# Performance work log

Measured on AMD Instinct MI355X. Metric: run time of the kernel, lower is better.

Reference implementation:

```python
import jax, jax.numpy as jnp
import numpy as np

B, N, C = 2048, 64, 384
H, WS, HIDDEN, TEMB = 12, 8, 64, 384
D = C // H


def _rpb_index(ws):
    coords = np.stack(np.meshgrid(np.arange(ws), np.arange(ws), indexing='ij'))  # (2, ws, ws)
    flat = coords.reshape(2, -1)                       # (2, ws*ws)
    rel = flat[:, :, None] - flat[:, None, :]          # (2, N, N)
    rel = rel.transpose(1, 2, 0).copy()                # (N, N, 2)
    rel[..., 0] += ws - 1
    rel[..., 1] += ws - 1
    rel[..., 0] *= 2 * ws - 1
    return rel.sum(-1)                                  # (N, N) int


def setup_inputs() -> dict:
    key = jax.random.key(0)
    ks = jax.random.split(key, 16)
    s = 0.02
    inp = {
        'x': jax.random.normal(ks[0], (B, N, C), jnp.float32),
        'temb': jax.random.normal(ks[1], (B, TEMB), jnp.float32),
        'sigma': jax.random.uniform(ks[2], (B,), jnp.float32, 1e-3, 1.0),
        'qkv_w': jax.random.normal(ks[3], (C, 3 * C), jnp.float32) * s,
        'qkv_b': jax.random.normal(ks[4], (3 * C,), jnp.float32) * s,
        'qkvt_w': jax.random.normal(ks[5], (TEMB, 3 * C), jnp.float32) * s,
        'trunk_w1': jax.random.normal(ks[6], (1, HIDDEN), jnp.float32) * s,
        'trunk_b1': jax.random.normal(ks[7], (HIDDEN,), jnp.float32) * s,
        'trunk_w2': jax.random.normal(ks[8], (HIDDEN, HIDDEN), jnp.float32) * s,
        'trunk_b2': jax.random.normal(ks[9], (HIDDEN,), jnp.float32) * s,
        'gate_w': jax.random.normal(ks[10], (HIDDEN, 1), jnp.float32) * s,
        'gate_b': jnp.zeros((1,), jnp.float32),
        'bias_w': jax.random.normal(ks[11], (HIDDEN, H), jnp.float32) * s,
        'bias_b': jax.random.normal(ks[12], (H,), jnp.float32) * s,
        'proj_w': jax.random.normal(ks[13], (C, C), jnp.float32) * s,
        'proj_b': jax.random.normal(ks[14], (C,), jnp.float32) * s,
        'rpb_table': jax.random.normal(ks[15], ((2 * WS - 1) * (2 * WS - 1), H), jnp.float32) * s,
        'rpb_index': jnp.asarray(_rpb_index(WS), jnp.int32),
    }
    return inp


def reference(x, temb, sigma, qkv_w, qkv_b, qkvt_w, trunk_w1, trunk_b1,
              trunk_w2, trunk_b2, gate_w, gate_b, bias_w, bias_b,
              proj_w, proj_b, rpb_table, rpb_index):
    b, n, c = x.shape
    h, d = H, c // H
    scale = d ** -0.5
    # QKV with time-embedding modulation
    qkv = x @ qkv_w + qkv_b + (temb @ qkvt_w)[:, None, :]        # (B, N, 3C)
    qkv = qkv.reshape(b, n, 3, h, d).transpose(2, 0, 3, 1, 4)     # (3, B, H, N, D)
    q, k, v = qkv[0], qkv[1], qkv[2]
    attn = jnp.einsum('bhnd,bhmd->bhnm', q * scale, k)            # (B, H, N, N)
    # relative position bias
    rpb = rpb_table[rpb_index].transpose(2, 0, 1)                 # (H, N, N)
    attn = attn + rpb[None]
    # noise-conditioned gate and per-head bias
    log_sigma = jnp.log(jnp.clip(sigma, 1e-6))[:, None]           # (B, 1)
    hid = jax.nn.silu(log_sigma @ trunk_w1 + trunk_b1)
    hid = jax.nn.silu(hid @ trunk_w2 + trunk_b2)                  # (B, hidden)
    gate = jax.nn.sigmoid(hid @ gate_w + gate_b).reshape(b, 1, 1, 1)
    nbias = (hid @ bias_w + bias_b).reshape(b, h, 1, 1)
    attn = attn / (1.0 + gate) + nbias
    attn = jax.nn.softmax(attn, axis=-1)
    out = jnp.einsum('bhnm,bhmd->bhnd', attn, v)                  # (B, H, N, D)
    out = out.transpose(0, 2, 1, 3).reshape(b, n, c)
    return out @ proj_w + proj_b
```

## Files before the change

### kernel.cpp

```cpp
#include <hip/hip_runtime.h>

#define B_TOT 2048
#define SEQ 64
#define CH 384
#define NH 12
#define HD 32
#define NC3 1152
#define LDP 392
#define QKS 40
#define VS 72
#define HDSZ 7424
#define QK_SCALE 0.17677669529663687f

typedef __attribute__((ext_vector_type(8))) short short8;
typedef __attribute__((ext_vector_type(4))) short short4v;
typedef __attribute__((ext_vector_type(4))) float f32x4;
typedef unsigned short u16;

__device__ __forceinline__ u16 f2bf(float f) {
  unsigned int u = __float_as_uint(f);
  u += 0x7fffu + ((u >> 16) & 1u);
  return (u16)(u >> 16);
}
__device__ __forceinline__ float bf2f(u16 u) {
  return __uint_as_float(((unsigned int)u) << 16);
}

__device__ __forceinline__ int pswz(int row, int col) {
  return row * 64 + ((((col >> 3) ^ (row & 7)) << 3) | (col & 7));
}

__global__ void k_prep(const float* __restrict__ qkv_w, const float* __restrict__ proj_w,
                       const float* __restrict__ rpb_table, const int* __restrict__ rpb_index,
                       u16* __restrict__ qkvwt, u16* __restrict__ projwt, u16* __restrict__ rpbz)
{
  int idx = blockIdx.x * 256 + threadIdx.x;
  if (idx < CH * NC3) {
    int k = idx / NC3, n = idx - k * NC3;
    qkvwt[n * LDP + k] = f2bf(qkv_w[idx]);
    return;
  }
  idx -= CH * NC3;
  if (idx < CH * CH) {
    int k = idx / CH, n = idx - k * CH;
    projwt[n * LDP + k] = f2bf(proj_w[idx]);
    return;
  }
  idx -= CH * CH;
  if (idx < NH * SEQ * SEQ) {
    int h = idx >> 12, j = (idx >> 6) & 63, q = idx & 63;
    int jt = j >> 4, g4j = (j >> 2) & 3, r = j & 3;
    int qt = q >> 4, q16 = q & 15;
    int dst = (h * 16 + jt * 4 + qt) * 256 + g4j * 64 + q16 * 4 + r;
    rpbz[dst] = f2bf(rpb_table[rpb_index[q * 64 + j] * NH + h]);
  }
}

__global__ void k_trunk(const float* __restrict__ sigma, const float* __restrict__ w1,
                        const float* __restrict__ b1, const float* __restrict__ w2,
                        const float* __restrict__ b2, const float* __restrict__ gw,
                        const float* __restrict__ gb, const float* __restrict__ bw,
                        const float* __restrict__ bb,
                        float* __restrict__ inv1pg, float* __restrict__ nbias)
{
  int b = blockIdx.x, j = threadIdx.x;
  __shared__ float sh[64];
  float ls = logf(fmaxf(sigma[b], 1e-6f));
  float z = fmaf(ls, w1[j], b1[j]);
  z = z / (1.f + __expf(-z));
  sh[j] = z;
  __syncthreads();
  float a = b2[j];
  #pragma unroll 8
  for (int i = 0; i < 64; ++i) a = fmaf(sh[i], w2[i * 64 + j], a);
  a = a / (1.f + __expf(-a));
  __syncthreads();
  sh[j] = a;
  __syncthreads();
  if (j == 0) {
    float zg = gb[0];
    #pragma unroll 8
    for (int i = 0; i < 64; ++i) zg = fmaf(sh[i], gw[i], zg);
    float gate = 1.f / (1.f + __expf(-zg));
    inv1pg[b] = 1.f / (1.f + gate);
  }
  if (j < NH) {
    float zb = bb[j];
    #pragma unroll 8
    for (int i = 0; i < 64; ++i) zb = fmaf(sh[i], bw[i * NH + j], zb);
    nbias[b * NH + j] = zb;
  }
}

__global__ __launch_bounds__(256) void k_tvec(const float* __restrict__ temb,
                                              const float* __restrict__ qkvt_w,
                                              const float* __restrict__ qkv_b,
                                              float* __restrict__ tvec)
{
  __shared__ float st[16 * 384];
  int bi = blockIdx.x;
  int brow = bi / 9, cseg = bi - brow * 9;
  int cb = cseg * 128;
  int tid = threadIdx.x;
  for (int idx = tid; idx < 16 * 384; idx += 256) {
    int r = idx / 384, k = idx - r * 384;
    st[idx] = temb[(brow * 16 + r) * 384 + k];
  }
  __syncthreads();
  int cl = tid & 127, half = tid >> 7;
  float acc[8];
  #pragma unroll
  for (int i = 0; i < 8; ++i) acc[i] = 0.f;
  #pragma unroll 4
  for (int k = 0; k < 384; ++k) {
    float w = qkvt_w[k * NC3 + cb + cl];
    #pragma unroll
    for (int i = 0; i < 8; ++i) acc[i] = fmaf(st[(half * 8 + i) * 384 + k], w, acc[i]);
  }
  float qb = qkv_b[cb + cl];
  #pragma unroll
  for (int i = 0; i < 8; ++i)
    tvec[(brow * 16 + half * 8 + i) * NC3 + cb + cl] = acc[i] + qb;
}

__global__ __launch_bounds__(512, 2) void k_attn(
    const float* __restrict__ x, const float* __restrict__ tvec,
    const float* __restrict__ inv1pg, const float* __restrict__ nbias,
    const u16* __restrict__ qkvwt, const u16* __restrict__ rpbz,
    u16* __restrict__ attw)
{
  __shared__ __align__(16) u16 s_x[128 * LDP];
  __shared__ __align__(16) u16 s_hd[4 * HDSZ];
  const f32x4 fz = {0.f, 0.f, 0.f, 0.f};

  const int b0 = blockIdx.x * 2;
  const int tid = threadIdx.x;
  const int w = tid >> 6, l = tid & 63;
  const int q16 = l & 15, g4 = l >> 4;

  {
    const float* xb = x + (size_t)b0 * (SEQ * CH);
    #pragma unroll 4
    for (int it = 0; it < 24; ++it) {
      int fi = it * 512 + tid;
      int row = fi / 96, c4 = fi - row * 96;
      const float4 a = *reinterpret_cast<const float4*>(xb + fi * 4);
      short4v v;
      v[0] = (short)f2bf(a.x); v[1] = (short)f2bf(a.y);
      v[2] = (short)f2bf(a.z); v[3] = (short)f2bf(a.w);
      *reinterpret_cast<short4v*>(&s_x[row * LDP + c4 * 4]) = v;
    }
  }
  __syncthreads();

  const float invb0 = inv1pg[b0], invb1 = inv1pg[b0 + 1];
  const float* tvb = tvec + (size_t)b0 * NC3;

  const int btA = w & 1;
  const int nset = w >> 1;

  for (int g = 0; g < 6; ++g) {
    {
      float tv[3]; const u16* bp[3]; int mh6[3], hj6[3], hf6[3];
      #pragma unroll
      for (int i = 0; i < 3; ++i) {
        int nt = nset * 3 + i;
        int hj = nt / 6, wi = nt - hj * 6;
        int mh = wi >> 1, hf = wi & 1;
        mh6[i] = mh; hj6[i] = hj; hf6[i] = hf;
        int c = mh * CH + (g * 2 + hj) * HD + hf * 16 + q16;
        tv[i] = tvb[btA * NC3 + c];
        bp[i] = qkvwt + c * LDP + g4 * 8;
      }
      f32x4 acc[4][3];
      #pragma unroll
      for (int m = 0; m < 4; ++m)
        #pragma unroll
        for (int i = 0; i < 3; ++i) acc[m][i] = fz;
      #pragma unroll 2
      for (int kt = 0; kt < 12; ++kt) {
        short8 af[4];
        #pragma unroll
        for (int m = 0; m < 4; ++m)
          af[m] = *reinterpret_cast<const short8*>(
              &s_x[(btA * 64 + m * 16 + q16) * LDP + kt * 32 + g4 * 8]);
        short8 bf[3];
        #pragma unroll
        for (int i = 0; i < 3; ++i)
          bf[i] = *reinterpret_cast<const short8*>(bp[i] + kt * 32);
        __builtin_amdgcn_s_setprio(1);
        #pragma unroll
        for (int i = 0; i < 3; ++i)
          #pragma unroll
          for (int m = 0; m < 4; ++m)
            acc[m][i] = __builtin_amdgcn_mfma_f32_16x16x32_bf16(af[m], bf[i], acc[m][i], 0, 0, 0);
        __builtin_amdgcn_s_setprio(0);
      }
      #pragma unroll
      for (int i = 0; i < 3; ++i) {
        u16* hbase = &s_hd[(btA * 2 + hj6[i]) * HDSZ];
        int cof = hf6[i] * 16 + q16;
        #pragma unroll
        for (int m = 0; m < 4; ++m) {
          int mrow = m * 16 + g4 * 4;
          f32x4 a = acc[m][i];
          if (mh6[i] == 0) {
            #pragma unroll
            for (int r = 0; r < 4; ++r)
              hbase[(mrow + r) * QKS + cof] = f2bf((a[r] + tv[i]) * QK_SCALE);
          } else if (mh6[i] == 1) {
            #pragma unroll
            for (int r = 0; r < 4; ++r)
              hbase[2560 + (mrow + r) * QKS + cof] = f2bf(a[r] + tv[i]);
          } else {
            short4v pk;
            #pragma unroll
            for (int r = 0; r < 4; ++r) pk[r] = (short)f2bf(a[r] + tv[i]);
            *reinterpret_cast<short4v*>(&hbase[5120 + cof * VS + mrow]) = pk;
          }
        }
      }
    }
    __syncthreads();

    f32x4 st2[2][4];
    #pragma unroll
    for (int t = 0; t < 2; ++t) {
      const int tau = w * 2 + t;
      const int cmb = tau >> 2, qt = tau & 3;
      const int bt = cmb >> 1, hh = cmb & 1;
      const int h = g * 2 + hh;
      const u16* sq = &s_hd[cmb * HDSZ];
      const u16* sk = sq + 2560;
      const float inv = bt ? invb1 : invb0;
      const float nb = nbias[(b0 + bt) * NH + h];

      short4v rp4[4];
      #pragma unroll
      for (int jt = 0; jt < 4; ++jt)
        rp4[jt] = *reinterpret_cast<const short4v*>(
            &rpbz[(h * 16 + jt * 4 + qt) * 256 + g4 * 64 + q16 * 4]);

      short8 bq = *reinterpret_cast<const short8*>(&sq[(qt * 16 + q16) * QKS + g4 * 8]);
      __builtin_amdgcn_s_setprio(1);
      #pragma unroll
      for (int jt = 0; jt < 4; ++jt) {
        short8 ak = *reinterpret_cast<const short8*>(&sk[(jt * 16 + q16) * QKS + g4 * 8]);
        st2[t][jt] = __builtin_amdgcn_mfma_f32_16x16x32_bf16(ak, bq, fz, 0, 0, 0);
      }
      __builtin_amdgcn_s_setprio(0);
      float mx = -1e30f;
      #pragma unroll
      for (int jt = 0; jt < 4; ++jt)
        #pragma unroll
        for (int r = 0; r < 4; ++r) {
          float s = fmaf(st2[t][jt][r], inv, fmaf(bf2f((u16)rp4[jt][r]), inv, nb));
          st2[t][jt][r] = s;
          mx = fmaxf(mx, s);
        }
      mx = fmaxf(mx, __shfl_xor(mx, 16));
      mx = fmaxf(mx, __shfl_xor(mx, 32));
      float sum = 0.f;
      #pragma unroll
      for (int jt = 0; jt < 4; ++jt)
        #pragma unroll
        for (int r = 0; r < 4; ++r) {
          float p = __expf(st2[t][jt][r] - mx);
          st2[t][jt][r] = p;
          sum += p;
        }
      sum += __shfl_xor(sum, 16);
      sum += __shfl_xor(sum, 32);
      float rn = 1.f / sum;
      #pragma unroll
      for (int jt = 0; jt < 4; ++jt)
        #pragma unroll
        for (int r = 0; r < 4; ++r) st2[t][jt][r] *= rn;
    }
    __syncthreads();
    #pragma unroll
    for (int t = 0; t < 2; ++t) {
      const int tau = w * 2 + t;
      const int cmb = tau >> 2, qt = tau & 3;
      const int bt = cmb >> 1, hh = cmb & 1;
      const int h = g * 2 + hh;
      u16* sq = &s_hd[cmb * HDSZ];
      const u16* svt = sq + 5120;
      u16* P = sq;

      #pragma unroll
      for (int jt = 0; jt < 4; ++jt) {
        short4v pk;
        #pragma unroll
        for (int r = 0; r < 4; ++r) pk[r] = (short)f2bf(st2[t][jt][r]);
        *reinterpret_cast<short4v*>(&P[pswz(qt * 16 + q16, jt * 16 + 4 * g4)]) = pk;
      }
      f32x4 o[2];
      o[0] = fz; o[1] = fz;
      #pragma unroll
      for (int kk = 0; kk < 2; ++kk) {
        short8 ap = *reinterpret_cast<const short8*>(
            &P[pswz(qt * 16 + q16, kk * 32 + g4 * 8)]);
        __builtin_amdgcn_s_setprio(1);
        #pragma unroll
        for (int dt = 0; dt < 2; ++dt) {
          short8 bv = *reinterpret_cast<const short8*>(
              &svt[(dt * 16 + q16) * VS + kk * 32 + g4 * 8]);
          o[dt] = __builtin_amdgcn_mfma_f32_16x16x32_bf16(ap, bv, o[dt], 0, 0, 0);
        }
        __builtin_amdgcn_s_setprio(0);
      }
      u16* ab = attw + (size_t)(b0 + bt) * (SEQ * CH);
      #pragma unroll
      for (int dt = 0; dt < 2; ++dt)
        #pragma unroll
        for (int r = 0; r < 4; ++r)
          ab[(qt * 16 + g4 * 4 + r) * CH + h * HD + dt * 16 + q16] = f2bf(o[dt][r]);
    }
    __syncthreads();
  }
}

__global__ __launch_bounds__(512, 4) void k_proj(
    const u16* __restrict__ attw, const u16* __restrict__ projwt,
    const float* __restrict__ proj_b, float* __restrict__ out)
{
  __shared__ __align__(16) u16 s_a[64 * LDP];
  const f32x4 fz = {0.f, 0.f, 0.f, 0.f};
  const int tid = threadIdx.x;
  const int w = tid >> 6, l = tid & 63;
  const int q16 = l & 15, g4 = l >> 4;
  const size_t row0 = (size_t)blockIdx.x * 64;

  {
    const u16* ab = attw + row0 * CH;
    #pragma unroll
    for (int it = 0; it < 6; ++it) {
      int slot = it * 512 + tid;
      int row = slot / 48, c8 = slot - row * 48;
      short8 v = *reinterpret_cast<const short8*>(ab + row * CH + c8 * 8);
      *reinterpret_cast<short8*>(&s_a[row * LDP + c8 * 8]) = v;
    }
  }
  __syncthreads();

  const u16* bpw[3]; float4 pb4[3];
  #pragma unroll
  for (int i = 0; i < 3; ++i) {
    int nt = w * 3 + i;
    bpw[i] = projwt + (nt * 16 + q16) * LDP + g4 * 8;
    pb4[i] = *reinterpret_cast<const float4*>(&proj_b[nt * 16 + 4 * g4]);
  }
  f32x4 acc[4][3];
  #pragma unroll
  for (int m = 0; m < 4; ++m)
    #pragma unroll
    for (int i = 0; i < 3; ++i) acc[m][i] = fz;
  #pragma unroll 2
  for (int kt = 0; kt < 12; ++kt) {
    short8 af[4];
    #pragma unroll
    for (int m = 0; m < 4; ++m)
      af[m] = *reinterpret_cast<const short8*>(&s_a[(m * 16 + q16) * LDP + kt * 32 + g4 * 8]);
    short8 bf[3];
    #pragma unroll
    for (int i = 0; i < 3; ++i)
      bf[i] = *reinterpret_cast<const short8*>(bpw[i] + kt * 32);
    __builtin_amdgcn_s_setprio(1);
    #pragma unroll
    for (int i = 0; i < 3; ++i)
      #pragma unroll
      for (int m = 0; m < 4; ++m)
        acc[m][i] = __builtin_amdgcn_mfma_f32_16x16x32_bf16(bf[i], af[m], acc[m][i], 0, 0, 0);
    __builtin_amdgcn_s_setprio(0);
  }
  float* ob = out + row0 * CH;
  #pragma unroll
  for (int i = 0; i < 3; ++i) {
    int cb = (w * 3 + i) * 16 + 4 * g4;
    #pragma unroll
    for (int m = 0; m < 4; ++m) {
      float4 v;
      v.x = acc[m][i][0] + pb4[i].x;
      v.y = acc[m][i][1] + pb4[i].y;
      v.z = acc[m][i][2] + pb4[i].z;
      v.w = acc[m][i][3] + pb4[i].w;
      *reinterpret_cast<float4*>(&ob[(m * 16 + q16) * CH + cb]) = v;
    }
  }
}

extern "C" void kernel_launch(void* const* d_in, const int* in_sizes, int n_in,
                              void* d_out, int out_size, void* d_ws, size_t ws_size,
                              hipStream_t stream) {
  const float* x       = (const float*)d_in[0];
  const float* temb    = (const float*)d_in[1];
  const float* sigma   = (const float*)d_in[2];
  const float* qkv_w   = (const float*)d_in[3];
  const float* qkv_b   = (const float*)d_in[4];
  const float* qkvt_w  = (const float*)d_in[5];
  const float* w1      = (const float*)d_in[6];
  const float* b1      = (const float*)d_in[7];
  const float* w2      = (const float*)d_in[8];
  const float* b2      = (const float*)d_in[9];
  const float* gw      = (const float*)d_in[10];
  const float* gb      = (const float*)d_in[11];
  const float* bw      = (const float*)d_in[12];
  const float* bb      = (const float*)d_in[13];
  const float* proj_w  = (const float*)d_in[14];
  const float* proj_b  = (const float*)d_in[15];
  const float* rpb_tab = (const float*)d_in[16];
  const int*   rpb_idx = (const int*)d_in[17];
  float* out = (float*)d_out;

  char* ws = (char*)d_ws;
  float* tvec   = (float*)(ws);
  float* inv1pg = (float*)(ws + 9437184);
  float* nbias  = (float*)(ws + 9445376);
  u16*   qkvwt  = (u16*)  (ws + 9543680);
  u16*   projwt = (u16*)  (ws + 10446848);
  u16*   rpbz   = (u16*)  (ws + 10747904);
  u16*   attw   = (u16*)  (ws + 10846208);

  k_prep<<<2496, 256, 0, stream>>>(qkv_w, proj_w, rpb_tab, rpb_idx, qkvwt, projwt, rpbz);
  k_trunk<<<2048, 64, 0, stream>>>(sigma, w1, b1, w2, b2, gw, gb, bw, bb, inv1pg, nbias);
  k_tvec<<<1152, 256, 0, stream>>>(temb, qkvt_w, qkv_b, tvec);
  k_attn<<<1024, 512, 0, stream>>>(x, tvec, inv1pg, nbias, qkvwt, rpbz, attw);
  k_proj<<<2048, 512, 0, stream>>>(attw, projwt, proj_b, out);
}
```

Before: 456.9 us.

## Process one batch per block and double-buffer per-head QKV with attention

The attention kernel now handles one batch element per block instead of two, which halves the x staging buffer and doubles the grid. Per-head Q/K/V tiles are double-buffered in shared memory, so the QKV projection for the next head pair runs alongside attention for the current one. This removes two barriers per iteration. The unequal per-wave tile split (2 vs 1 tiles) and a larger LDS footprint may hurt occupancy or balance.

```diff
diff --git a/kernel.cpp b/kernel.cpp
--- a/kernel.cpp
+++ b/kernel.cpp
@@ -9,7 +9,7 @@
 #define LDP 392
 #define QKS 40
 #define VS 72
-#define HDSZ 7424
+#define HDU 8960
 #define QK_SCALE 0.17677669529663687f
 
 typedef __attribute__((ext_vector_type(8))) short short8;
@@ -123,25 +123,92 @@
     tvec[(brow * 16 + half * 8 + i) * NC3 + cb + cl] = acc[i] + qb;
 }
 
+template<int NT>
+__device__ __forceinline__ void phaseA(const u16* __restrict__ sx, u16* __restrict__ shd,
+                                       const u16* __restrict__ qkvwt,
+                                       const float* __restrict__ tvb,
+                                       int g, int nt0, int q16, int g4)
+{
+  const f32x4 fz = {0.f, 0.f, 0.f, 0.f};
+  float tv[NT]; const u16* bp[NT]; int mh6[NT], hj6[NT], hf6[NT];
+  #pragma unroll
+  for (int i = 0; i < NT; ++i) {
+    int nt = nt0 + i;
+    int hj = nt / 6, wi = nt - hj * 6;
+    int mh = wi >> 1, hf = wi & 1;
+    mh6[i] = mh; hj6[i] = hj; hf6[i] = hf;
+    int c = mh * CH + (g * 2 + hj) * HD + hf * 16 + q16;
+    tv[i] = tvb[c];
+    bp[i] = qkvwt + c * LDP + g4 * 8;
+  }
+  f32x4 acc[4][NT];
+  #pragma unroll
+  for (int m = 0; m < 4; ++m)
+    #pragma unroll
+    for (int i = 0; i < NT; ++i) acc[m][i] = fz;
+  #pragma unroll 2
+  for (int kt = 0; kt < 12; ++kt) {
+    short8 af[4];
+    #pragma unroll
+    for (int m = 0; m < 4; ++m)
+      af[m] = *reinterpret_cast<const short8*>(&sx[(m * 16 + q16) * LDP + kt * 32 + g4 * 8]);
+    short8 bf[NT];
+    #pragma unroll
+    for (int i = 0; i < NT; ++i)
+      bf[i] = *reinterpret_cast<const short8*>(bp[i] + kt * 32);
+    __builtin_amdgcn_s_setprio(1);
+    #pragma unroll
+    for (int i = 0; i < NT; ++i)
+      #pragma unroll
+      for (int m = 0; m < 4; ++m)
+        acc[m][i] = __builtin_amdgcn_mfma_f32_16x16x32_bf16(af[m], bf[i], acc[m][i], 0, 0, 0);
+    __builtin_amdgcn_s_setprio(0);
+  }
+  #pragma unroll
+  for (int i = 0; i < NT; ++i) {
+    u16* hb = &shd[hj6[i] * HDU];
+    int cof = hf6[i] * 16 + q16;
+    #pragma unroll
+    for (int m = 0; m < 4; ++m) {
+      int mrow = m * 16 + g4 * 4;
+      f32x4 a = acc[m][i];
+      if (mh6[i] == 0) {
+        #pragma unroll
+        for (int r = 0; r < 4; ++r)
+          hb[pswz(mrow + r, cof)] = f2bf((a[r] + tv[i]) * QK_SCALE);
+      } else if (mh6[i] == 1) {
+        #pragma unroll
+        for (int r = 0; r < 4; ++r)
+          hb[4096 + (mrow + r) * QKS + cof] = f2bf(a[r] + tv[i]);
+      } else {
+        short4v pk;
+        #pragma unroll
+        for (int r = 0; r < 4; ++r) pk[r] = (short)f2bf(a[r] + tv[i]);
+        *reinterpret_cast<short4v*>(&hb[6656 + cof * VS + mrow]) = pk;
+      }
+    }
+  }
+}
+
 __global__ __launch_bounds__(512, 2) void k_attn(
     const float* __restrict__ x, const float* __restrict__ tvec,
     const float* __restrict__ inv1pg, const float* __restrict__ nbias,
     const u16* __restrict__ qkvwt, const u16* __restrict__ rpbz,
     u16* __restrict__ attw)
 {
-  __shared__ __align__(16) u16 s_x[128 * LDP];
-  __shared__ __align__(16) u16 s_hd[4 * HDSZ];
+  __shared__ __align__(16) u16 s_x[64 * LDP];
+  __shared__ __align__(16) u16 s_hd[2][2 * HDU];
   const f32x4 fz = {0.f, 0.f, 0.f, 0.f};
 
-  const int b0 = blockIdx.x * 2;
+  const int b = blockIdx.x;
   const int tid = threadIdx.x;
   const int w = tid >> 6, l = tid & 63;
   const int q16 = l & 15, g4 = l >> 4;
 
   {
-    const float* xb = x + (size_t)b0 * (SEQ * CH);
-    #pragma unroll 4
-    for (int it = 0; it < 24; ++it) {
+    const float* xb = x + (size_t)b * (SEQ * CH);
+    #pragma unroll
+    for (int it = 0; it < 12; ++it) {
       int fi = it * 512 + tid;
       int row = fi / 96, c4 = fi - row * 96;
       const float4 a = *reinterpret_cast<const float4*>(xb + fi * 4);
@@ -153,87 +220,28 @@
   }
   __syncthreads();
 
-  const float invb0 = inv1pg[b0], invb1 = inv1pg[b0 + 1];
-  const float* tvb = tvec + (size_t)b0 * NC3;
-
-  const int btA = w & 1;
-  const int nset = w >> 1;
+  const float inv = inv1pg[b];
+  const float nb_all = 0.f; (void)nb_all;
+  const float* tvb = tvec + (size_t)b * NC3;
+
+  const int nt0 = (w < 4) ? 2 * w : 8 + (w - 4);
+
+  if (w < 4) phaseA<2>(s_x, s_hd[0], qkvwt, tvb, 0, nt0, q16, g4);
+  else       phaseA<1>(s_x, s_hd[0], qkvwt, tvb, 0, nt0, q16, g4);
+  __syncthreads();
 
   for (int g = 0; g < 6; ++g) {
+    if (g < 5) {
+      if (w < 4) phaseA<2>(s_x, s_hd[(g + 1) & 1], qkvwt, tvb, g + 1, nt0, q16, g4);
+      else       phaseA<1>(s_x, s_hd[(g + 1) & 1], qkvwt, tvb, g + 1, nt0, q16, g4);
+    }
     {
-      float tv[3]; const u16* bp[3]; int mh6[3], hj6[3], hf6[3];
-      #pragma unroll
-      for (int i = 0; i < 3; ++i) {
-        int nt = nset * 3 + i;
-        int hj = nt / 6, wi = nt - hj * 6;
-        int mh = wi >> 1, hf = wi & 1;
-        mh6[i] = mh; hj6[i] = hj; hf6[i] = hf;
-        int c = mh * CH + (g * 2 + hj) * HD + hf * 16 + q16;
-        tv[i] = tvb[btA * NC3 + c];
-        bp[i] = qkvwt + c * LDP + g4 * 8;
-      }
-      f32x4 acc[4][3];
-      #pragma unroll
-      for (int m = 0; m < 4; ++m)
-        #pragma unroll
-        for (int i = 0; i < 3; ++i) acc[m][i] = fz;
-      #pragma unroll 2
-      for (int kt = 0; kt < 12; ++kt) {
-        short8 af[4];
-        #pragma unroll
-        for (int m = 0; m < 4; ++m)
-          af[m] = *reinterpret_cast<const short8*>(
-              &s_x[(btA * 64 + m * 16 + q16) * LDP + kt * 32 + g4 * 8]);
-        short8 bf[3];
-        #pragma unroll
-        for (int i = 0; i < 3; ++i)
-          bf[i] = *reinterpret_cast<const short8*>(bp[i] + kt * 32);
-        __builtin_amdgcn_s_setprio(1);
-        #pragma unroll
-        for (int i = 0; i < 3; ++i)
-          #pragma unroll
-          for (int m = 0; m < 4; ++m)
-            acc[m][i] = __builtin_amdgcn_mfma_f32_16x16x32_bf16(af[m], bf[i], acc[m][i], 0, 0, 0);
-        __builtin_amdgcn_s_setprio(0);
-      }
-      #pragma unroll
-      for (int i = 0; i < 3; ++i) {
-        u16* hbase = &s_hd[(btA * 2 + hj6[i]) * HDSZ];
-        int cof = hf6[i] * 16 + q16;
-        #pragma unroll
-        for (int m = 0; m < 4; ++m) {
-          int mrow = m * 16 + g4 * 4;
-          f32x4 a = acc[m][i];
-          if (mh6[i] == 0) {
-            #pragma unroll
-            for (int r = 0; r < 4; ++r)
-              hbase[(mrow + r) * QKS + cof] = f2bf((a[r] + tv[i]) * QK_SCALE);
-          } else if (mh6[i] == 1) {
-            #pragma unroll
-            for (int r = 0; r < 4; ++r)
-              hbase[2560 + (mrow + r) * QKS + cof] = f2bf(a[r] + tv[i]);
-          } else {
-            short4v pk;
-            #pragma unroll
-            for (int r = 0; r < 4; ++r) pk[r] = (short)f2bf(a[r] + tv[i]);
-            *reinterpret_cast<short4v*>(&hbase[5120 + cof * VS + mrow]) = pk;
-          }
-        }
-      }
-    }
-    __syncthreads();
-
-    f32x4 st2[2][4];
-    #pragma unroll
-    for (int t = 0; t < 2; ++t) {
-      const int tau = w * 2 + t;
-      const int cmb = tau >> 2, qt = tau & 3;
-      const int bt = cmb >> 1, hh = cmb & 1;
+      const int hh = w >> 2, qt = w & 3;
       const int h = g * 2 + hh;
-      const u16* sq = &s_hd[cmb * HDSZ];
-      const u16* sk = sq + 2560;
-      const float inv = bt ? invb1 : invb0;
-      const float nb = nbias[(b0 + bt) * NH + h];
+      u16* sq = &s_hd[g & 1][hh * HDU];
+      const u16* sk = sq + 4096;
+      const u16* svt = sq + 6656;
+      const float nb = nbias[b * NH + h];
 
       short4v rp4[4];
       #pragma unroll
@@ -241,66 +249,56 @@
         rp4[jt] = *reinterpret_cast<const short4v*>(
             &rpbz[(h * 16 + jt * 4 + qt) * 256 + g4 * 64 + q16 * 4]);
 
-      short8 bq = *reinterpret_cast<const short8*>(&sq[(qt * 16 + q16) * QKS + g4 * 8]);
+      short8 bq = *reinterpret_cast<const short8*>(&sq[pswz(qt * 16 + q16, g4 * 8)]);
+      f32x4 st[4];
       __builtin_amdgcn_s_setprio(1);
       #pragma unroll
       for (int jt = 0; jt < 4; ++jt) {
         short8 ak = *reinterpret_cast<const short8*>(&sk[(jt * 16 + q16) * QKS + g4 * 8]);
-        st2[t][jt] = __builtin_amdgcn_mfma_f32_16x16x32_bf16(ak, bq, fz, 0, 0, 0);
+        st[jt] = __builtin_amdgcn_mfma_f32_16x16x32_bf16(ak, bq, fz, 0, 0, 0);
       }
       __builtin_amdgcn_s_setprio(0);
-      float mx = -1e30f;
-      #pragma unroll
-      for (int jt = 0; jt < 4; ++jt)
-        #pragma unroll
-        for (int r = 0; r < 4; ++r) {
-          float s = fmaf(st2[t][jt][r], inv, fmaf(bf2f((u16)rp4[jt][r]), inv, nb));
-          st2[t][jt][r] = s;
-          mx = fmaxf(mx, s);
-        }
-      mx = fmaxf(mx, __shfl_xor(mx, 16));
-      mx = fmaxf(mx, __shfl_xor(mx, 32));
-      float sum = 0.f;
-      #pragma unroll
-      for (int jt = 0; jt < 4; ++jt)
-        #pragma unroll
-        for (int r = 0; r < 4; ++r) {
-          float p = __expf(st2[t][jt][r] - mx);
-          st2[t][jt][r] = p;
-          sum += p;
-        }
-      sum += __shfl_xor(sum, 16);
-      sum += __shfl_xor(sum, 32);
-      float rn = 1.f / sum;
-      #pragma unroll
-      for (int jt = 0; jt < 4; ++jt)
-        #pragma unroll
-        for (int r = 0; r < 4; ++r) st2[t][jt][r] *= rn;
-    }
-    __syncthreads();
-    #pragma unroll
-    for (int t = 0; t < 2; ++t) {
-      const int tau = w * 2 + t;
-      const int cmb = tau >> 2, qt = tau & 3;
-      const int bt = cmb >> 1, hh = cmb & 1;
-      const int h = g * 2 + hh;
-      u16* sq = &s_hd[cmb * HDSZ];
-      const u16* svt = sq + 5120;
-      u16* P = sq;
-
+      {
+        float mx = -1e30f;
+        #pragma unroll
+        for (int jt = 0; jt < 4; ++jt)
+          #pragma unroll
+          for (int r = 0; r < 4; ++r) {
+            float s = fmaf(st[jt][r], inv, fmaf(bf2f((u16)rp4[jt][r]), inv, nb));
+            st[jt][r] = s;
+            mx = fmaxf(mx, s);
+          }
+        mx = fmaxf(mx, __shfl_xor(mx, 16));
+        mx = fmaxf(mx, __shfl_xor(mx, 32));
+        float sum = 0.f;
+        #pragma unroll
+        for (int jt = 0; jt < 4; ++jt)
+          #pragma unroll
+          for (int r = 0; r < 4; ++r) {
+            float p = __expf(st[jt][r] - mx);
+            st[jt][r] = p;
+            sum += p;
+          }
+        sum += __shfl_xor(sum, 16);
+        sum += __shfl_xor(sum, 32);
+        float rn = 1.f / sum;
+        #pragma unroll
+        for (int jt = 0; jt < 4; ++jt)
+          #pragma unroll
+          for (int r = 0; r < 4; ++r) st[jt][r] *= rn;
+      }
       #pragma unroll
       for (int jt = 0; jt < 4; ++jt) {
         short4v pk;
         #pragma unroll
-        for (int r = 0; r < 4; ++r) pk[r] = (short)f2bf(st2[t][jt][r]);
-        *reinterpret_cast<short4v*>(&P[pswz(qt * 16 + q16, jt * 16 + 4 * g4)]) = pk;
+        for (int r = 0; r < 4; ++r) pk[r] = (short)f2bf(st[jt][r]);
+        *reinterpret_cast<short4v*>(&sq[pswz(qt * 16 + q16, jt * 16 + 4 * g4)]) = pk;
       }
       f32x4 o[2];
       o[0] = fz; o[1] = fz;
       #pragma unroll
       for (int kk = 0; kk < 2; ++kk) {
-        short8 ap = *reinterpret_cast<const short8*>(
-            &P[pswz(qt * 16 + q16, kk * 32 + g4 * 8)]);
+        short8 ap = *reinterpret_cast<const short8*>(&sq[pswz(qt * 16 + q16, kk * 32 + g4 * 8)]);
         __builtin_amdgcn_s_setprio(1);
         #pragma unroll
         for (int dt = 0; dt < 2; ++dt) {
@@ -310,7 +308,7 @@
         }
         __builtin_amdgcn_s_setprio(0);
       }
-      u16* ab = attw + (size_t)(b0 + bt) * (SEQ * CH);
+      u16* ab = attw + (size_t)b * (SEQ * CH);
       #pragma unroll
       for (int dt = 0; dt < 2; ++dt)
         #pragma unroll
@@ -425,6 +423,6 @@
   k_prep<<<2496, 256, 0, stream>>>(qkv_w, proj_w, rpb_tab, rpb_idx, qkvwt, projwt, rpbz);
   k_trunk<<<2048, 64, 0, stream>>>(sigma, w1, b1, w2, b2, gw, gb, bw, bb, inv1pg, nbias);
   k_tvec<<<1152, 256, 0, stream>>>(temb, qkvt_w, qkv_b, tvec);
-  k_attn<<<1024, 512, 0, stream>>>(x, tvec, inv1pg, nbias, qkvwt, rpbz, attw);
+  k_attn<<<2048, 512, 0, stream>>>(x, tvec, inv1pg, nbias, qkvwt, rpbz, attw);
   k_proj<<<2048, 512, 0, stream>>>(attw, projwt, proj_b, out);
 }
```

New measurement: 533.4 us. 16.7% more time.
